# Kernel optimization log

Hardware: AMD Instinct MI355X
Metric: run time of the kernel (lower is better)

Reference implementation:

```python
import jax, jax.numpy as jnp
import numpy as np

CURVE = 1.0
TAU = 0.5
N_NODES = 32768
N_EDGES = 65536
IN_CH = 64
OUT_CH = 64
N_HEADS = 8
N_RF = 128
EPS = 1e-7


def _make_projection_matrix(m, d, seed=0):
    # FAVOR+ projection: stacked rows of transposed QR blocks, row-rescaled by chi norms.
    rng = np.random.RandomState(seed)
    blocks = []
    nb_full = m // d
    for _ in range(nb_full):
        q, _ = np.linalg.qr(rng.randn(d, d))
        blocks.append(q.T)
    rem = m - nb_full * d
    if rem > 0:
        q, _ = np.linalg.qr(rng.randn(d, d))
        blocks.append(q.T[:rem])
    final = np.vstack(blocks)  # [m, d]
    mult = np.linalg.norm(rng.randn(m, d), axis=1)
    return (mult[:, None] * final).astype(np.float32)


def _expmap0(u, c):
    # Hyperboloid exp map at origin; time slot of u is ignored.
    sqrtK = 1.0 / jnp.sqrt(c)
    x = u[..., 1:]
    xn = jnp.maximum(jnp.linalg.norm(x, axis=-1, keepdims=True), EPS)
    theta = xn / sqrtK
    return jnp.concatenate([sqrtK * jnp.cosh(theta), sqrtK * jnp.sinh(theta) * x / xn], axis=-1)


def _proj(x, c):
    # Re-project onto hyperboloid: x0 = sqrt(1/c + ||x_space||^2)
    K = 1.0 / c
    y = x[..., 1:]
    t = jnp.sqrt(K + jnp.sum(y * y, axis=-1, keepdims=True))
    return jnp.concatenate([t, y], axis=-1)


def _logmap0(x, c):
    # Hyperboloid log map at origin; output tangent has zero time component.
    sqrtK = 1.0 / jnp.sqrt(c)
    y = x[..., 1:]
    yn = jnp.maximum(jnp.linalg.norm(y, axis=-1, keepdims=True), EPS)
    t = jnp.maximum(x[..., 0:1] / sqrtK, 1.0 + EPS)
    res = sqrtK * jnp.arccosh(t) * y / yn
    return jnp.concatenate([jnp.zeros_like(res[..., :1]), res], axis=-1)


def _softmax_kernel(data, P, tau, c):
    # Performer-style exp kernel with hyperbolic (time-coordinate) prefactor.
    dt = data[..., 0:1]
    ds = data[..., 1:]
    m = 1.0 / jnp.sqrt(jnp.asarray(P.shape[0], jnp.float32))
    wx = jnp.exp(jnp.einsum('bnhd,dm->bnhm', ds, P) / jnp.sqrt(tau))
    front = jnp.exp((c / tau - dt * dt / tau) / 2.0) * m  # [b,n,h,1]
    return wx * front


def setup_inputs() -> dict:
    key = jax.random.key(0)
    k1, k2, k3, k4 = jax.random.split(key, 4)
    std = (2.0 / (IN_CH + OUT_CH)) ** 0.5
    z = 0.01 * jax.random.normal(k1, (1, N_NODES, IN_CH), jnp.float32)
    Wq = std * jax.random.normal(k2, (N_HEADS, OUT_CH, IN_CH), jnp.float32)
    Wk = std * jax.random.normal(k3, (N_HEADS, OUT_CH, IN_CH), jnp.float32)
    Wv = std * jax.random.normal(k4, (N_HEADS, OUT_CH, IN_CH), jnp.float32)
    edge_index = jax.random.randint(jax.random.fold_in(key, 7), (2, N_EDGES), 0, N_NODES, jnp.int32)
    proj_mat = jnp.asarray(_make_projection_matrix(IN_CH - 1, N_RF))  # [63, 128]
    return {"z": z, "Wq": Wq, "Wk": Wk, "Wv": Wv, "proj_mat": proj_mat, "edge_index": edge_index}


def reference(z, Wq, Wk, Wv, proj_mat, edge_index):
    c = jnp.float32(CURVE)
    tau = jnp.float32(TAU)
    zs = z[0]  # [N, C] (B == 1, squeeze)
    zh = _proj(_expmap0(zs, c), c)  # lift features to hyperboloid
    u = _logmap0(zh, c)             # [N, C], tangent at origin

    def hyplin(W):  # HypLinear (no bias): proj(expmap0(logmap0(x) @ W^T)) for all heads
        mu = jnp.einsum('nc,hoc->hno', u, W)  # [H, N, D]
        return _proj(_expmap0(mu, c), c)

    q, k, v = hyplin(Wq), hyplin(Wk), hyplin(Wv)  # [H, N, D]
    H, N, D = q.shape
    # mirrors torch stacked.reshape(-1, N, H, D) (row-major relabeling)
    query = q.reshape(1, N, H, D)
    key_ = k.reshape(1, N, H, D)
    value = v.reshape(1, N, H, D)

    qp = _softmax_kernel(query, proj_mat, tau, c).transpose(2, 0, 1, 3)  # [H,1,N,M]
    kp = _softmax_kernel(key_, proj_mat, tau, c).transpose(2, 0, 1, 3)   # [H,1,N,M]
    vv = value.transpose(2, 0, 1, 3)                                      # [H,1,N,D]

    last = jnp.einsum('hbnm,hbnd->hbmd', kp, vv)   # [H,1,M,D] kv summary
    zo = jnp.einsum('hbnm,hbmd->hbnd', qp, last)   # [H,1,N,D]
    mnorm = -zo[..., 0:1] ** 2 + jnp.sum(zo[..., 1:] ** 2, axis=-1, keepdims=True)
    zo = zo / (jnp.sqrt(c) * jnp.sqrt(jnp.abs(mnorm)))  # renormalize onto hyperboloid

    start, end = edge_index[0], edge_index[1]
    ea = jnp.einsum('hbem,hbem->hbe', qp[:, :, end, :], kp[:, :, start, :])
    A_weight = ea.transpose(1, 2, 0)  # [1, E, H]

    # hyper_agg: Euclidean head-mean followed by Minkowski renormalization
    t = jnp.mean(zo[:, 0], axis=0)  # [N, D]
    xn = -t[..., 0:1] ** 2 + jnp.sum(t[..., 1:] ** 2, axis=-1, keepdims=True)
    z_next = t / (jnp.sqrt(c) * jnp.sqrt(jnp.abs(xn)))
    link_loss = jnp.mean(A_weight)
    return z_next, link_loss
```

## Files before the change

kernel.cpp:

```cpp
#include <hip/hip_runtime.h>

#define DEV __device__ __forceinline__

#define NNODES 32768
#define NEDGES 65536
#define NROWS  262144
#define EPSF   1e-7f
#define SQRT2F 1.4142135623730951f
#define LOG2E  1.4426950408889634f
#define LOG2SQRT63 2.9886399611087573f

#define OFF_WFRAG 0u
#define OFF_LASTB 0u
#define OFF_PFRAG 196608u
#define OFF_EA    212992u
#define OFF_U     409600u
#define OFF_PART  42352640u
#define OFF_PHIQ  75907072u
#define OFF_PHIK  143015936u

typedef short s8v __attribute__((ext_vector_type(8)));
typedef float f4v __attribute__((ext_vector_type(4)));
typedef float f2v __attribute__((ext_vector_type(2)));

DEV unsigned short f2bf(float f) {
  unsigned u = __float_as_uint(f);
  return (unsigned short)((u + 0x7fffu + ((u >> 16) & 1u)) >> 16);
}
DEV float bf2f(unsigned short h) { return __uint_as_float(((unsigned)h) << 16); }
DEV unsigned pack2(float lo, float hi) {
  return __builtin_amdgcn_perm(__float_as_uint(hi) + 0x8000u, __float_as_uint(lo) + 0x8000u, 0x07060302u);
}
DEV float frcp(float x) { return __builtin_amdgcn_rcpf(x); }

__global__ __launch_bounds__(256) void k01_prep(const float* __restrict__ z, unsigned short* __restrict__ ubf,
                                                const float* __restrict__ Wq, const float* __restrict__ Wk,
                                                const float* __restrict__ Wv, const float* __restrict__ P,
                                                unsigned short* __restrict__ Wfrag, unsigned short* __restrict__ Pfrag,
                                                float* __restrict__ ea) {
  int i = blockIdx.x * 256 + threadIdx.x;
  float4 v = *(const float4*)(z + (size_t)i * 4);
  if ((i & 15) == 0) v.x = 0.f;
  uint2 pk;
  pk.x = pack2(v.x, v.y);
  pk.y = pack2(v.z, v.w);
  *(uint2*)(ubf + (size_t)i * 4) = pk;

  if (blockIdx.x < 96) {
    if (i == 0) ea[0] = 0.f;
    int stride = 96 * 256;
    for (int t = i; t < 98304; t += stride) {
      int j = t & 7, lane = (t >> 3) & 63, nt = (t >> 9) & 3, ks = (t >> 11) & 1, h = (t >> 12) & 7, sm = t >> 15;
      int k = ks * 32 + (lane >> 4) * 8 + j;
      int n = nt * 16 + (lane & 15);
      const float* W = (sm == 0) ? Wq : ((sm == 1) ? Wk : Wv);
      Wfrag[t] = f2bf(W[(h * 64 + n) * 64 + k]);
    }
    for (int t = i; t < 8192; t += stride) {
      int j = t & 7, lane = (t >> 3) & 63, ks = (t >> 9) & 1, mt = (t >> 10) & 7;
      int k = ks * 32 + (lane >> 4) * 8 + j;
      int m = mt * 16 + (lane & 15);
      Pfrag[t] = (k == 0) ? (unsigned short)0 : f2bf(P[(k - 1) * 128 + m] * (SQRT2F * LOG2E));
    }
  }
}

__global__ __launch_bounds__(256) void k2_mfma(const unsigned short* __restrict__ ubf,
                                               const unsigned short* __restrict__ Wfrag,
                                               const unsigned short* __restrict__ Pfrag,
                                               unsigned char* __restrict__ phiq, unsigned char* __restrict__ phik,
                                               unsigned short* __restrict__ part) {
  __shared__ short lds_raw[18944];
  short* sbuf = lds_raw;
  float* sfront = (float*)(lds_raw + 18432);
  short* kbufT = lds_raw;
  short* vbufT = lds_raw + 8704;

  int w = threadIdx.x >> 6, lane = threadIdx.x & 63;
  int q = lane >> 4, l = lane & 15;
  int b = blockIdx.x;
  int h = b >> 8, t = b & 255;
  int n0 = t * 128 + w * 32;
  int r0 = h * 32768 + n0;

  s8v afr[2][2];
#pragma unroll
  for (int mt = 0; mt < 2; ++mt)
#pragma unroll
    for (int ks = 0; ks < 2; ++ks)
      afr[mt][ks] = *(const s8v*)(ubf + (size_t)(n0 + mt * 16 + l) * 64 + ks * 32 + q * 8);

  const s8v* Wf = (const s8v*)Wfrag;
  const s8v* Pf = (const s8v*)Pfrag;
  uint2 vkeep[2][4];

#pragma unroll
  for (int sm = 0; sm < 3; ++sm) {
    f4v acc[2][4];
#pragma unroll
    for (int mt = 0; mt < 2; ++mt)
#pragma unroll
      for (int nt = 0; nt < 4; ++nt) acc[mt][nt] = (f4v)(0.f);
#pragma unroll
    for (int ks = 0; ks < 2; ++ks)
#pragma unroll
      for (int nt = 0; nt < 4; ++nt) {
        s8v bf = Wf[(((sm * 8 + h) * 2 + ks) * 4 + nt) * 64 + lane];
#pragma unroll
        for (int mt = 0; mt < 2; ++mt)
          acc[mt][nt] = __builtin_amdgcn_mfma_f32_16x16x32_bf16(afr[mt][ks], bf, acc[mt][nt], 0, 0, 0);
      }
#pragma unroll
    for (int mt = 0; mt < 2; ++mt) {
      float rs[4];
#pragma unroll
      for (int reg = 0; reg < 4; ++reg) {
        float v0 = (l == 0) ? 0.f : acc[mt][0][reg];
        rs[reg] = v0 * v0 + acc[mt][1][reg] * acc[mt][1][reg] + acc[mt][2][reg] * acc[mt][2][reg] +
                  acc[mt][3][reg] * acc[mt][3][reg];
      }
#pragma unroll
      for (int reg = 0; reg < 4; ++reg) {
#pragma unroll
        for (int off = 1; off < 16; off <<= 1) rs[reg] += __shfl_xor(rs[reg], off, 64);
      }
      float vreg[4][4];
#pragma unroll
      for (int reg = 0; reg < 4; ++reg) {
        float x = fmaxf(sqrtf(rs[reg]), EPSF);
        float e = exp2f(x * LOG2E);
        float sh = 0.5f * (e - frcp(e));
        float ratio = sh * frcp(x);
        float sh2 = sh * sh;
        int row = mt * 16 + q * 4 + reg;
        if (sm == 2) {
          float tt2 = sqrtf(1.f + sh2);
#pragma unroll
          for (int nt = 0; nt < 4; ++nt) {
            float val = acc[mt][nt][reg] * ratio;
            if (l == 0 && nt == 0) val = tt2;
            vreg[nt][reg] = val;
          }
        } else {
          float lf = -sh2 * LOG2E - LOG2SQRT63;
          if (l == 0) sfront[(sm * 4 + w) * 32 + row] = lf;
#pragma unroll
          for (int nt = 0; nt < 4; ++nt) {
            float val = acc[mt][nt][reg] * ratio;
            if (l == 0 && nt == 0) val = 0.f;
            sbuf[(sm * 4 + w) * 2304 + row * 72 + nt * 16 + l] = (short)(__float_as_uint(val) >> 16);
          }
        }
      }
      if (sm == 2) {
#pragma unroll
        for (int nt = 0; nt < 4; ++nt) {
          vkeep[mt][nt].x = pack2(vreg[nt][0], vreg[nt][1]);
          vkeep[mt][nt].y = pack2(vreg[nt][2], vreg[nt][3]);
        }
      }
    }
  }

  uint2 keep0[8], keep1[8];
#pragma unroll
  for (int sm = 0; sm < 2; ++sm) {
    s8v bsf[2][2];
#pragma unroll
    for (int nt = 0; nt < 2; ++nt)
#pragma unroll
      for (int ks = 0; ks < 2; ++ks)
        bsf[nt][ks] = *(const s8v*)&sbuf[(sm * 4 + w) * 2304 + (nt * 16 + l) * 72 + ks * 32 + q * 8];
    float lf0 = sfront[(sm * 4 + w) * 32 + l];
    float lf1 = sfront[(sm * 4 + w) * 32 + 16 + l];
    unsigned char* dst = sm ? phik : phiq;
#pragma unroll
    for (int mt = 0; mt < 8; ++mt) {
      f4v a0 = (f4v)(0.f), a1 = (f4v)(0.f);
#pragma unroll
      for (int ks = 0; ks < 2; ++ks) {
        s8v ap = Pf[(mt * 2 + ks) * 64 + lane];
        a0 = __builtin_amdgcn_mfma_f32_16x16x32_bf16(ap, bsf[0][ks], a0, 0, 0, 0);
        a1 = __builtin_amdgcn_mfma_f32_16x16x32_bf16(ap, bsf[1][ks], a1, 0, 0, 0);
      }
      float v00 = exp2f(a0[0] + lf0), v01 = exp2f(a0[1] + lf0), v02 = exp2f(a0[2] + lf0), v03 = exp2f(a0[3] + lf0);
      float v10 = exp2f(a1[0] + lf1), v11 = exp2f(a1[1] + lf1), v12 = exp2f(a1[2] + lf1), v13 = exp2f(a1[3] + lf1);
      unsigned p0 = __builtin_amdgcn_cvt_pk_fp8_f32(v00, v01, 0, 0);
      p0 = __builtin_amdgcn_cvt_pk_fp8_f32(v02, v03, p0, 1);
      unsigned p1 = __builtin_amdgcn_cvt_pk_fp8_f32(v10, v11, 0, 0);
      p1 = __builtin_amdgcn_cvt_pk_fp8_f32(v12, v13, p1, 1);
      *(unsigned*)(dst + (size_t)(r0 + l) * 128 + mt * 16 + q * 4) = p0;
      *(unsigned*)(dst + (size_t)(r0 + 16 + l) * 128 + mt * 16 + q * 4) = p1;
      if (sm == 1) {
        keep0[mt].x = pack2(v00, v01); keep0[mt].y = pack2(v02, v03);
        keep1[mt].x = pack2(v10, v11); keep1[mt].y = pack2(v12, v13);
      }
    }
  }

  f4v facc[2][4];
#pragma unroll
  for (int mtl = 0; mtl < 2; ++mtl)
#pragma unroll
    for (int nt = 0; nt < 4; ++nt) facc[mtl][nt] = (f4v)(0.f);

#pragma unroll
  for (int hf = 0; hf < 2; ++hf) {
    __syncthreads();
    if ((w >> 1) == hf) {
      int nd0 = (w & 1) * 32 + l, nd1 = nd0 + 16;
#pragma unroll
      for (int mt = 0; mt < 8; ++mt) {
        int m = mt * 16 + q * 4;
        kbufT[(m + 0) * 68 + nd0] = (short)(keep0[mt].x & 0xffffu);
        kbufT[(m + 1) * 68 + nd0] = (short)(keep0[mt].x >> 16);
        kbufT[(m + 2) * 68 + nd0] = (short)(keep0[mt].y & 0xffffu);
        kbufT[(m + 3) * 68 + nd0] = (short)(keep0[mt].y >> 16);
        kbufT[(m + 0) * 68 + nd1] = (short)(keep1[mt].x & 0xffffu);
        kbufT[(m + 1) * 68 + nd1] = (short)(keep1[mt].x >> 16);
        kbufT[(m + 2) * 68 + nd1] = (short)(keep1[mt].y & 0xffffu);
        kbufT[(m + 3) * 68 + nd1] = (short)(keep1[mt].y >> 16);
      }
#pragma unroll
      for (int mt = 0; mt < 2; ++mt)
#pragma unroll
        for (int nt = 0; nt < 4; ++nt)
          *(uint2*)&vbufT[(nt * 16 + l) * 72 + (w & 1) * 32 + mt * 16 + q * 4] = vkeep[mt][nt];
    }
    __syncthreads();
#pragma unroll
    for (int kc = 0; kc < 2; ++kc) {
      s8v bv[4];
#pragma unroll
      for (int nt = 0; nt < 4; ++nt)
        bv[nt] = *(const s8v*)&vbufT[(nt * 16 + l) * 72 + kc * 32 + q * 8];
      s8v av[2];
#pragma unroll
      for (int mtl = 0; mtl < 2; ++mtl) {
        const short* kb = &kbufT[((2 * w + mtl) * 16 + l) * 68 + kc * 32 + q * 8];
        union { s8v v; long long L[2]; } ua;
        ua.L[0] = *(const long long*)kb;
        ua.L[1] = *(const long long*)(kb + 4);
        av[mtl] = ua.v;
      }
#pragma unroll
      for (int mtl = 0; mtl < 2; ++mtl)
#pragma unroll
        for (int nt = 0; nt < 4; ++nt)
          facc[mtl][nt] = __builtin_amdgcn_mfma_f32_16x16x32_bf16(av[mtl], bv[nt], facc[mtl][nt], 0, 0, 0);
    }
  }

#pragma unroll
  for (int mtl = 0; mtl < 2; ++mtl)
#pragma unroll
    for (int nt = 0; nt < 4; ++nt) {
      uint2 pk;
      pk.x = pack2(facc[mtl][nt][0], facc[mtl][nt][1]);
      pk.y = pack2(facc[mtl][nt][2], facc[mtl][nt][3]);
      int d = nt * 16 + l;
      int m = (2 * w + mtl) * 16 + q * 4;
      *(uint2*)(part + ((size_t)((t * 8 + h) * 64 + d)) * 128 + m) = pk;
    }
}

__global__ __launch_bounds__(256) void k3p_pack(const unsigned* __restrict__ part32, unsigned char* __restrict__ lastB) {
  int t2 = blockIdx.x * 256 + threadIdx.x;
  float s0 = 0.f, s1 = 0.f;
#pragma unroll 16
  for (int c = 0; c < 256; ++c) {
    unsigned v = part32[((size_t)c << 12) + t2];
    s0 += __uint_as_float(v << 16);
    s1 += __uint_as_float(v & 0xffff0000u);
  }
  int m = (t2 & 63) * 2, d = (t2 >> 6) & 63, h = t2 >> 12;
  int ks = m >> 5, j = m & 7, qq = (m >> 3) & 3;
  int lane = qq * 16 + (d & 15), nt = d >> 4;
  unsigned r = __builtin_amdgcn_cvt_pk_bf8_f32(s0, s1, 0, 0);
  *(unsigned short*)(lastB + ((((h * 4 + ks) * 4 + nt) * 64 + lane) << 3) + j) = (unsigned short)r;
}

__global__ __launch_bounds__(512) void k4_mfma(const unsigned char* __restrict__ phiq,
                                               const unsigned char* __restrict__ lastB,
                                               const float* __restrict__ ea, float* __restrict__ out) {
  __shared__ unsigned zbufT[8][64][18];
  int w = threadIdx.x >> 6, lane = threadIdx.x & 63;
  int q = lane >> 4, l = lane & 15;
  int n0 = blockIdx.x * 32;

  const long* Bf = (const long*)lastB;
  long bf[4][4];
#pragma unroll
  for (int ks = 0; ks < 4; ++ks)
#pragma unroll
    for (int nt = 0; nt < 4; ++nt) bf[ks][nt] = Bf[((w * 4 + ks) * 4 + nt) * 64 + lane];

  long af[2][4];
#pragma unroll
  for (int mt = 0; mt < 2; ++mt)
#pragma unroll
    for (int ks = 0; ks < 4; ++ks)
      af[mt][ks] = *(const long*)(phiq + (size_t)(8 * (n0 + mt * 16 + l) + w) * 128 + ks * 32 + q * 8);

  f4v acc[2][4];
#pragma unroll
  for (int mt = 0; mt < 2; ++mt)
#pragma unroll
    for (int nt = 0; nt < 4; ++nt) acc[mt][nt] = (f4v)(0.f);
#pragma unroll
  for (int ks = 0; ks < 4; ++ks)
#pragma unroll
    for (int nt = 0; nt < 4; ++nt)
#pragma unroll
      for (int mt = 0; mt < 2; ++mt)
        acc[mt][nt] = __builtin_amdgcn_mfma_f32_16x16x32_fp8_bf8(af[mt][ks], bf[ks][nt], acc[mt][nt], 0, 0, 0);

#pragma unroll
  for (int mt = 0; mt < 2; ++mt) {
    float rs[4];
#pragma unroll
    for (int reg = 0; reg < 4; ++reg) {
      float v0 = acc[mt][0][reg];
      float s0 = (l == 0) ? -v0 * v0 : v0 * v0;
      rs[reg] = s0 + acc[mt][1][reg] * acc[mt][1][reg] + acc[mt][2][reg] * acc[mt][2][reg] +
                acc[mt][3][reg] * acc[mt][3][reg];
    }
#pragma unroll
    for (int reg = 0; reg < 4; ++reg) {
#pragma unroll
      for (int off = 1; off < 16; off <<= 1) rs[reg] += __shfl_xor(rs[reg], off, 64);
    }
    float inv[4];
#pragma unroll
    for (int reg = 0; reg < 4; ++reg) inv[reg] = 1.f / sqrtf(fabsf(rs[reg]));
#pragma unroll
    for (int nt = 0; nt < 4; ++nt) {
      uint2 pk;
      pk.x = pack2(acc[mt][nt][0] * inv[0], acc[mt][nt][1] * inv[1]);
      pk.y = pack2(acc[mt][nt][2] * inv[2], acc[mt][nt][3] * inv[3]);
      *(uint2*)&zbufT[w][nt * 16 + l][mt * 8 + q * 2] = pk;
    }
  }
  __syncthreads();

  int tid = threadIdx.x;
  int i = tid >> 4, dg = tid & 15;
  int i2 = i >> 1, sel = i & 1;
  float s[4] = {0.f, 0.f, 0.f, 0.f};
#pragma unroll
  for (int w2 = 0; w2 < 8; ++w2) {
#pragma unroll
    for (int j = 0; j < 4; ++j) {
      unsigned u = zbufT[w2][dg * 4 + j][i2];
      s[j] += bf2f((unsigned short)(sel ? (u >> 16) : (u & 0xffffu)));
    }
  }
  float m2 = 0.f;
#pragma unroll
  for (int j = 0; j < 4; ++j) {
    s[j] *= 0.125f;
    m2 += ((dg == 0 && j == 0) ? -s[j] * s[j] : s[j] * s[j]);
  }
#pragma unroll
  for (int off = 1; off < 16; off <<= 1) m2 += __shfl_xor(m2, off, 64);
  float inv = 1.f / sqrtf(fabsf(m2));
  float4 o = make_float4(s[0] * inv, s[1] * inv, s[2] * inv, s[3] * inv);
  *(float4*)(out + (size_t)(n0 + i) * 64 + dg * 4) = o;
  if (blockIdx.x == 0 && tid == 0) out[(size_t)NNODES * 64] = ea[0] * (1.0f / 524288.0f);
}

__global__ __launch_bounds__(256) void k5_ea(const unsigned char* __restrict__ phiq,
                                             const unsigned char* __restrict__ phik,
                                             const int* __restrict__ ei, float* __restrict__ ea) {
  __shared__ float part[4];
  int lane = threadIdx.x & 63, w = threadIdx.x >> 6;
  int wid = blockIdx.x * 4 + w;
  float acc = 0.f;
  for (int i = 0; i < 16; ++i) {
    int e = wid * 16 + i;
    int s = ei[e];
    int d = ei[NEDGES + e];
    uint4 qa = *(const uint4*)(phiq + (size_t)d * 1024 + lane * 16);
    uint4 ka = *(const uint4*)(phik + (size_t)s * 1024 + lane * 16);
    unsigned qs[4] = {qa.x, qa.y, qa.z, qa.w};
    unsigned ks[4] = {ka.x, ka.y, ka.z, ka.w};
#pragma unroll
    for (int p = 0; p < 4; ++p) {
      f2v q0 = __builtin_amdgcn_cvt_pk_f32_fp8(qs[p], 0);
      f2v q1 = __builtin_amdgcn_cvt_pk_f32_fp8(qs[p], 1);
      f2v k0 = __builtin_amdgcn_cvt_pk_f32_fp8(ks[p], 0);
      f2v k1 = __builtin_amdgcn_cvt_pk_f32_fp8(ks[p], 1);
      acc = fmaf(q0.x, k0.x, acc);
      acc = fmaf(q0.y, k0.y, acc);
      acc = fmaf(q1.x, k1.x, acc);
      acc = fmaf(q1.y, k1.y, acc);
    }
  }
#pragma unroll
  for (int o = 1; o < 64; o <<= 1) acc += __shfl_xor(acc, o, 64);
  if (lane == 0) part[w] = acc;
  __syncthreads();
  if (threadIdx.x == 0) atomicAdd(ea, part[0] + part[1] + part[2] + part[3]);
}

extern "C" void kernel_launch(void* const* d_in, const int* in_sizes, int n_in,
                              void* d_out, int out_size, void* d_ws, size_t ws_size,
                              hipStream_t stream) {
  const float* z  = (const float*)d_in[0];
  const float* Wq = (const float*)d_in[1];
  const float* Wk = (const float*)d_in[2];
  const float* Wv = (const float*)d_in[3];
  const float* P  = (const float*)d_in[4];
  const int* ei   = (const int*)d_in[5];
  char* ws = (char*)d_ws;
  unsigned short* Wfrag = (unsigned short*)(ws + OFF_WFRAG);
  unsigned char*  lastB = (unsigned char*)(ws + OFF_LASTB);
  unsigned short* Pfrag = (unsigned short*)(ws + OFF_PFRAG);
  float*          ea    = (float*)(ws + OFF_EA);
  unsigned short* ubf   = (unsigned short*)(ws + OFF_U);
  unsigned short* part  = (unsigned short*)(ws + OFF_PART);
  unsigned char*  phiq  = (unsigned char*)(ws + OFF_PHIQ);
  unsigned char*  phik  = (unsigned char*)(ws + OFF_PHIK);

  k01_prep<<<2048, 256, 0, stream>>>(z, ubf, Wq, Wk, Wv, P, Wfrag, Pfrag, ea);
  k2_mfma<<<2048, 256, 0, stream>>>(ubf, Wfrag, Pfrag, phiq, phik, part);
  k3p_pack<<<128, 256, 0, stream>>>((const unsigned*)part, lastB);
  k5_ea<<<NEDGES / 64, 256, 0, stream>>>(phiq, phik, ei, ea);
  k4_mfma<<<NNODES / 32, 512, 0, stream>>>(phiq, lastB, ea, (float*)d_out);
}
```

Measured before the change: 201.9 us.

## Merge partial-sum pack and edge-score kernels into one launch, use fast intrinsics

Combines the k3p_pack reduction and the k5_ea edge dot-product kernels into a single launch with block ranges split by index, so the two independent stages run concurrently and one launch is removed. The edge part now gives each wave 8 edges instead of 16, using twice as many blocks, and loads two edges per iteration with split accumulators for more memory-level parallelism. Library sqrtf, exp2f and division are replaced with raw AMDGCN sqrt, exp2 and rcp intrinsics, trading a little accuracy and denormal handling for fewer instructions.

```diff
diff --git a/kernel.cpp b/kernel.cpp
--- a/kernel.cpp
+++ b/kernel.cpp
@@ -32,6 +32,8 @@
   return __builtin_amdgcn_perm(__float_as_uint(hi) + 0x8000u, __float_as_uint(lo) + 0x8000u, 0x07060302u);
 }
 DEV float frcp(float x) { return __builtin_amdgcn_rcpf(x); }
+DEV float fsqrt(float x) { return __builtin_amdgcn_sqrtf(x); }
+DEV float fexp2(float x) { return __builtin_amdgcn_exp2f(x); }
 
 __global__ __launch_bounds__(256) void k01_prep(const float* __restrict__ z, unsigned short* __restrict__ ubf,
                                                 const float* __restrict__ Wq, const float* __restrict__ Wk,
@@ -127,14 +129,14 @@
       float vreg[4][4];
 #pragma unroll
       for (int reg = 0; reg < 4; ++reg) {
-        float x = fmaxf(sqrtf(rs[reg]), EPSF);
-        float e = exp2f(x * LOG2E);
+        float x = fmaxf(fsqrt(rs[reg]), EPSF);
+        float e = fexp2(x * LOG2E);
         float sh = 0.5f * (e - frcp(e));
         float ratio = sh * frcp(x);
         float sh2 = sh * sh;
         int row = mt * 16 + q * 4 + reg;
         if (sm == 2) {
-          float tt2 = sqrtf(1.f + sh2);
+          float tt2 = fsqrt(1.f + sh2);
 #pragma unroll
           for (int nt = 0; nt < 4; ++nt) {
             float val = acc[mt][nt][reg] * ratio;
@@ -183,8 +185,8 @@
         a0 = __builtin_amdgcn_mfma_f32_16x16x32_bf16(ap, bsf[0][ks], a0, 0, 0, 0);
         a1 = __builtin_amdgcn_mfma_f32_16x16x32_bf16(ap, bsf[1][ks], a1, 0, 0, 0);
       }
-      float v00 = exp2f(a0[0] + lf0), v01 = exp2f(a0[1] + lf0), v02 = exp2f(a0[2] + lf0), v03 = exp2f(a0[3] + lf0);
-      float v10 = exp2f(a1[0] + lf1), v11 = exp2f(a1[1] + lf1), v12 = exp2f(a1[2] + lf1), v13 = exp2f(a1[3] + lf1);
+      float v00 = fexp2(a0[0] + lf0), v01 = fexp2(a0[1] + lf0), v02 = fexp2(a0[2] + lf0), v03 = fexp2(a0[3] + lf0);
+      float v10 = fexp2(a1[0] + lf1), v11 = fexp2(a1[1] + lf1), v12 = fexp2(a1[2] + lf1), v13 = fexp2(a1[3] + lf1);
       unsigned p0 = __builtin_amdgcn_cvt_pk_fp8_f32(v00, v01, 0, 0);
       p0 = __builtin_amdgcn_cvt_pk_fp8_f32(v02, v03, p0, 1);
       unsigned p1 = __builtin_amdgcn_cvt_pk_fp8_f32(v10, v11, 0, 0);
@@ -264,20 +266,59 @@
     }
 }
 
-__global__ __launch_bounds__(256) void k3p_pack(const unsigned* __restrict__ part32, unsigned char* __restrict__ lastB) {
-  int t2 = blockIdx.x * 256 + threadIdx.x;
-  float s0 = 0.f, s1 = 0.f;
+__global__ __launch_bounds__(256) void k35(const unsigned* __restrict__ part32, unsigned char* __restrict__ lastB,
+                                           const unsigned char* __restrict__ phiq,
+                                           const unsigned char* __restrict__ phik,
+                                           const int* __restrict__ ei, float* __restrict__ ea) {
+  int b = blockIdx.x;
+  if (b < 128) {
+    int t2 = b * 256 + threadIdx.x;
+    float s0 = 0.f, s1 = 0.f;
 #pragma unroll 16
-  for (int c = 0; c < 256; ++c) {
-    unsigned v = part32[((size_t)c << 12) + t2];
-    s0 += __uint_as_float(v << 16);
-    s1 += __uint_as_float(v & 0xffff0000u);
-  }
-  int m = (t2 & 63) * 2, d = (t2 >> 6) & 63, h = t2 >> 12;
-  int ks = m >> 5, j = m & 7, qq = (m >> 3) & 3;
-  int lane = qq * 16 + (d & 15), nt = d >> 4;
-  unsigned r = __builtin_amdgcn_cvt_pk_bf8_f32(s0, s1, 0, 0);
-  *(unsigned short*)(lastB + ((((h * 4 + ks) * 4 + nt) * 64 + lane) << 3) + j) = (unsigned short)r;
+    for (int c = 0; c < 256; ++c) {
+      unsigned v = part32[((size_t)c << 12) + t2];
+      s0 += __uint_as_float(v << 16);
+      s1 += __uint_as_float(v & 0xffff0000u);
+    }
+    int m = (t2 & 63) * 2, d = (t2 >> 6) & 63, h = t2 >> 12;
+    int ks = m >> 5, j = m & 7, qq = (m >> 3) & 3;
+    int lane = qq * 16 + (d & 15), nt = d >> 4;
+    unsigned r = __builtin_amdgcn_cvt_pk_bf8_f32(s0, s1, 0, 0);
+    *(unsigned short*)(lastB + ((((h * 4 + ks) * 4 + nt) * 64 + lane) << 3) + j) = (unsigned short)r;
+    return;
+  }
+  __shared__ float part[4];
+  int lane = threadIdx.x & 63, w = threadIdx.x >> 6;
+  int wid = (b - 128) * 4 + w;
+  float acc0 = 0.f, acc1 = 0.f;
+#pragma unroll
+  for (int i = 0; i < 8; i += 2) {
+    int e0 = wid * 8 + i, e1 = e0 + 1;
+    int s0 = ei[e0], d0 = ei[NEDGES + e0];
+    int s1 = ei[e1], d1 = ei[NEDGES + e1];
+    uint4 qa = *(const uint4*)(phiq + (size_t)d0 * 1024 + lane * 16);
+    uint4 ka = *(const uint4*)(phik + (size_t)s0 * 1024 + lane * 16);
+    uint4 qb = *(const uint4*)(phiq + (size_t)d1 * 1024 + lane * 16);
+    uint4 kb = *(const uint4*)(phik + (size_t)s1 * 1024 + lane * 16);
+    unsigned qs[8] = {qa.x, qa.y, qa.z, qa.w, qb.x, qb.y, qb.z, qb.w};
+    unsigned ks[8] = {ka.x, ka.y, ka.z, ka.w, kb.x, kb.y, kb.z, kb.w};
+#pragma unroll
+    for (int p = 0; p < 8; ++p) {
+      f2v q0 = __builtin_amdgcn_cvt_pk_f32_fp8(qs[p], 0);
+      f2v q1 = __builtin_amdgcn_cvt_pk_f32_fp8(qs[p], 1);
+      f2v k0 = __builtin_amdgcn_cvt_pk_f32_fp8(ks[p], 0);
+      f2v k1 = __builtin_amdgcn_cvt_pk_f32_fp8(ks[p], 1);
+      float t0 = fmaf(q0.x, k0.x, q0.y * k0.y);
+      float t1 = fmaf(q1.x, k1.x, q1.y * k1.y);
+      if (p < 4) acc0 += t0 + t1; else acc1 += t0 + t1;
+    }
+  }
+  float acc = acc0 + acc1;
+#pragma unroll
+  for (int o = 1; o < 64; o <<= 1) acc += __shfl_xor(acc, o, 64);
+  if (lane == 0) part[w] = acc;
+  __syncthreads();
+  if (threadIdx.x == 0) atomicAdd(ea, part[0] + part[1] + part[2] + part[3]);
 }
 
 __global__ __launch_bounds__(512) void k4_mfma(const unsigned char* __restrict__ phiq,
@@ -332,7 +373,7 @@
     }
     float inv[4];
 #pragma unroll
-    for (int reg = 0; reg < 4; ++reg) inv[reg] = 1.f / sqrtf(fabsf(rs[reg]));
+    for (int reg = 0; reg < 4; ++reg) inv[reg] = frcp(fsqrt(fabsf(rs[reg])));
 #pragma unroll
     for (int nt = 0; nt < 4; ++nt) {
       uint2 pk;
@@ -363,44 +404,10 @@
   }
 #pragma unroll
   for (int off = 1; off < 16; off <<= 1) m2 += __shfl_xor(m2, off, 64);
-  float inv = 1.f / sqrtf(fabsf(m2));
+  float inv = frcp(fsqrt(fabsf(m2)));
   float4 o = make_float4(s[0] * inv, s[1] * inv, s[2] * inv, s[3] * inv);
   *(float4*)(out + (size_t)(n0 + i) * 64 + dg * 4) = o;
   if (blockIdx.x == 0 && tid == 0) out[(size_t)NNODES * 64] = ea[0] * (1.0f / 524288.0f);
-}
-
-__global__ __launch_bounds__(256) void k5_ea(const unsigned char* __restrict__ phiq,
-                                             const unsigned char* __restrict__ phik,
-                                             const int* __restrict__ ei, float* __restrict__ ea) {
-  __shared__ float part[4];
-  int lane = threadIdx.x & 63, w = threadIdx.x >> 6;
-  int wid = blockIdx.x * 4 + w;
-  float acc = 0.f;
-  for (int i = 0; i < 16; ++i) {
-    int e = wid * 16 + i;
-    int s = ei[e];
-    int d = ei[NEDGES + e];
-    uint4 qa = *(const uint4*)(phiq + (size_t)d * 1024 + lane * 16);
-    uint4 ka = *(const uint4*)(phik + (size_t)s * 1024 + lane * 16);
-    unsigned qs[4] = {qa.x, qa.y, qa.z, qa.w};
-    unsigned ks[4] = {ka.x, ka.y, ka.z, ka.w};
-#pragma unroll
-    for (int p = 0; p < 4; ++p) {
-      f2v q0 = __builtin_amdgcn_cvt_pk_f32_fp8(qs[p], 0);
-      f2v q1 = __builtin_amdgcn_cvt_pk_f32_fp8(qs[p], 1);
-      f2v k0 = __builtin_amdgcn_cvt_pk_f32_fp8(ks[p], 0);
-      f2v k1 = __builtin_amdgcn_cvt_pk_f32_fp8(ks[p], 1);
-      acc = fmaf(q0.x, k0.x, acc);
-      acc = fmaf(q0.y, k0.y, acc);
-      acc = fmaf(q1.x, k1.x, acc);
-      acc = fmaf(q1.y, k1.y, acc);
-    }
-  }
-#pragma unroll
-  for (int o = 1; o < 64; o <<= 1) acc += __shfl_xor(acc, o, 64);
-  if (lane == 0) part[w] = acc;
-  __syncthreads();
-  if (threadIdx.x == 0) atomicAdd(ea, part[0] + part[1] + part[2] + part[3]);
 }
 
 extern "C" void kernel_launch(void* const* d_in, const int* in_sizes, int n_in,
@@ -424,7 +431,6 @@
 
   k01_prep<<<2048, 256, 0, stream>>>(z, ubf, Wq, Wk, Wv, P, Wfrag, Pfrag, ea);
   k2_mfma<<<2048, 256, 0, stream>>>(ubf, Wfrag, Pfrag, phiq, phik, part);
-  k3p_pack<<<128, 256, 0, stream>>>((const unsigned*)part, lastB);
-  k5_ea<<<NEDGES / 64, 256, 0, stream>>>(phiq, phik, ei, ea);
+  k35<<<128 + 2048, 256, 0, stream>>>((const unsigned*)part, lastB, phiq, phik, ei, ea);
   k4_mfma<<<NNODES / 32, 512, 0, stream>>>(phiq, lastB, ea, (float*)d_out);
 }
```

Result: faster. 194.0 us (-3.9%).

## Fuse edge-score and output kernels into one launch with last-block finalize

Applied to the files above, without the earlier changes.

Merges the edge attention-sum kernel and the output kernel into a single launch: the first 2048 blocks compute edge dot products, and the remaining blocks do the output MFMA work. The last edge block writes the link loss, detected through an atomic counter. The aim is to save a launch and let the two independent workloads overlap on the GPU. It also swaps library sqrt/exp2 calls for hardware intrinsics and raises the unroll factor in the pack kernel. In exchange it adds an extra atomic counter and relies on a threadfence for ordering.

```diff
diff --git a/kernel.cpp b/kernel.cpp
--- a/kernel.cpp
+++ b/kernel.cpp
@@ -32,6 +32,8 @@
   return __builtin_amdgcn_perm(__float_as_uint(hi) + 0x8000u, __float_as_uint(lo) + 0x8000u, 0x07060302u);
 }
 DEV float frcp(float x) { return __builtin_amdgcn_rcpf(x); }
+DEV float fsqrt(float x) { return __builtin_amdgcn_sqrtf(x); }
+DEV float fexp2(float x) { return __builtin_amdgcn_exp2f(x); }
 
 __global__ __launch_bounds__(256) void k01_prep(const float* __restrict__ z, unsigned short* __restrict__ ubf,
                                                 const float* __restrict__ Wq, const float* __restrict__ Wk,
@@ -47,7 +49,7 @@
   *(uint2*)(ubf + (size_t)i * 4) = pk;
 
   if (blockIdx.x < 96) {
-    if (i == 0) ea[0] = 0.f;
+    if (i == 0) { ea[0] = 0.f; ((unsigned*)ea)[1] = 0u; }
     int stride = 96 * 256;
     for (int t = i; t < 98304; t += stride) {
       int j = t & 7, lane = (t >> 3) & 63, nt = (t >> 9) & 3, ks = (t >> 11) & 1, h = (t >> 12) & 7, sm = t >> 15;
@@ -127,14 +129,14 @@
       float vreg[4][4];
 #pragma unroll
       for (int reg = 0; reg < 4; ++reg) {
-        float x = fmaxf(sqrtf(rs[reg]), EPSF);
-        float e = exp2f(x * LOG2E);
+        float x = fmaxf(fsqrt(rs[reg]), EPSF);
+        float e = fexp2(x * LOG2E);
         float sh = 0.5f * (e - frcp(e));
         float ratio = sh * frcp(x);
         float sh2 = sh * sh;
         int row = mt * 16 + q * 4 + reg;
         if (sm == 2) {
-          float tt2 = sqrtf(1.f + sh2);
+          float tt2 = fsqrt(1.f + sh2);
 #pragma unroll
           for (int nt = 0; nt < 4; ++nt) {
             float val = acc[mt][nt][reg] * ratio;
@@ -183,8 +185,8 @@
         a0 = __builtin_amdgcn_mfma_f32_16x16x32_bf16(ap, bsf[0][ks], a0, 0, 0, 0);
         a1 = __builtin_amdgcn_mfma_f32_16x16x32_bf16(ap, bsf[1][ks], a1, 0, 0, 0);
       }
-      float v00 = exp2f(a0[0] + lf0), v01 = exp2f(a0[1] + lf0), v02 = exp2f(a0[2] + lf0), v03 = exp2f(a0[3] + lf0);
-      float v10 = exp2f(a1[0] + lf1), v11 = exp2f(a1[1] + lf1), v12 = exp2f(a1[2] + lf1), v13 = exp2f(a1[3] + lf1);
+      float v00 = fexp2(a0[0] + lf0), v01 = fexp2(a0[1] + lf0), v02 = fexp2(a0[2] + lf0), v03 = fexp2(a0[3] + lf0);
+      float v10 = fexp2(a1[0] + lf1), v11 = fexp2(a1[1] + lf1), v12 = fexp2(a1[2] + lf1), v13 = fexp2(a1[3] + lf1);
       unsigned p0 = __builtin_amdgcn_cvt_pk_fp8_f32(v00, v01, 0, 0);
       p0 = __builtin_amdgcn_cvt_pk_fp8_f32(v02, v03, p0, 1);
       unsigned p1 = __builtin_amdgcn_cvt_pk_fp8_f32(v10, v11, 0, 0);
@@ -267,7 +269,7 @@
 __global__ __launch_bounds__(256) void k3p_pack(const unsigned* __restrict__ part32, unsigned char* __restrict__ lastB) {
   int t2 = blockIdx.x * 256 + threadIdx.x;
   float s0 = 0.f, s1 = 0.f;
-#pragma unroll 16
+#pragma unroll 32
   for (int c = 0; c < 256; ++c) {
     unsigned v = part32[((size_t)c << 12) + t2];
     s0 += __uint_as_float(v << 16);
@@ -280,13 +282,64 @@
   *(unsigned short*)(lastB + ((((h * 4 + ks) * 4 + nt) * 64 + lane) << 3) + j) = (unsigned short)r;
 }
 
-__global__ __launch_bounds__(512) void k4_mfma(const unsigned char* __restrict__ phiq,
-                                               const unsigned char* __restrict__ lastB,
-                                               const float* __restrict__ ea, float* __restrict__ out) {
+__global__ __launch_bounds__(512) void k45(const unsigned char* __restrict__ phiq,
+                                           const unsigned char* __restrict__ phik,
+                                           const unsigned char* __restrict__ lastB,
+                                           const int* __restrict__ ei,
+                                           float* __restrict__ ea, float* __restrict__ out) {
   __shared__ unsigned zbufT[8][64][18];
-  int w = threadIdx.x >> 6, lane = threadIdx.x & 63;
+  __shared__ float epart[8];
+  int b = blockIdx.x;
+  int lane = threadIdx.x & 63, w = threadIdx.x >> 6;
+
+  if (b < 2048) {
+    int wid = b * 8 + w;
+    int e0 = wid * 4;
+    int sA[4], dA[4];
+#pragma unroll
+    for (int j = 0; j < 4; ++j) { sA[j] = ei[e0 + j]; dA[j] = ei[NEDGES + e0 + j]; }
+    uint4 qv[4], kv[4];
+#pragma unroll
+    for (int j = 0; j < 4; ++j) {
+      qv[j] = *(const uint4*)(phiq + (size_t)dA[j] * 1024 + lane * 16);
+      kv[j] = *(const uint4*)(phik + (size_t)sA[j] * 1024 + lane * 16);
+    }
+    float acc = 0.f;
+#pragma unroll
+    for (int j = 0; j < 4; ++j) {
+      unsigned qs[4] = {qv[j].x, qv[j].y, qv[j].z, qv[j].w};
+      unsigned ks[4] = {kv[j].x, kv[j].y, kv[j].z, kv[j].w};
+#pragma unroll
+      for (int p = 0; p < 4; ++p) {
+        f2v q0 = __builtin_amdgcn_cvt_pk_f32_fp8(qs[p], 0);
+        f2v q1 = __builtin_amdgcn_cvt_pk_f32_fp8(qs[p], 1);
+        f2v k0 = __builtin_amdgcn_cvt_pk_f32_fp8(ks[p], 0);
+        f2v k1 = __builtin_amdgcn_cvt_pk_f32_fp8(ks[p], 1);
+        acc = fmaf(q0.x, k0.x, acc);
+        acc = fmaf(q0.y, k0.y, acc);
+        acc = fmaf(q1.x, k1.x, acc);
+        acc = fmaf(q1.y, k1.y, acc);
+      }
+    }
+#pragma unroll
+    for (int o = 1; o < 64; o <<= 1) acc += __shfl_xor(acc, o, 64);
+    if (lane == 0) epart[w] = acc;
+    __syncthreads();
+    if (threadIdx.x == 0) {
+      float bs = epart[0] + epart[1] + epart[2] + epart[3] + epart[4] + epart[5] + epart[6] + epart[7];
+      atomicAdd(ea, bs);
+      __threadfence();
+      unsigned prev = atomicAdd((unsigned*)(ea + 1), 1u);
+      if (prev == 2047u) {
+        float v = atomicAdd(ea, 0.f);
+        out[(size_t)NNODES * 64] = v * (1.0f / 524288.0f);
+      }
+    }
+    return;
+  }
+
   int q = lane >> 4, l = lane & 15;
-  int n0 = blockIdx.x * 32;
+  int n0 = (b - 2048) * 32;
 
   const long* Bf = (const long*)lastB;
   long bf[4][4];
@@ -332,7 +385,7 @@
     }
     float inv[4];
 #pragma unroll
-    for (int reg = 0; reg < 4; ++reg) inv[reg] = 1.f / sqrtf(fabsf(rs[reg]));
+    for (int reg = 0; reg < 4; ++reg) inv[reg] = frcp(fsqrt(fabsf(rs[reg])));
 #pragma unroll
     for (int nt = 0; nt < 4; ++nt) {
       uint2 pk;
@@ -363,44 +416,9 @@
   }
 #pragma unroll
   for (int off = 1; off < 16; off <<= 1) m2 += __shfl_xor(m2, off, 64);
-  float inv = 1.f / sqrtf(fabsf(m2));
+  float inv = frcp(fsqrt(fabsf(m2)));
   float4 o = make_float4(s[0] * inv, s[1] * inv, s[2] * inv, s[3] * inv);
   *(float4*)(out + (size_t)(n0 + i) * 64 + dg * 4) = o;
-  if (blockIdx.x == 0 && tid == 0) out[(size_t)NNODES * 64] = ea[0] * (1.0f / 524288.0f);
-}
-
-__global__ __launch_bounds__(256) void k5_ea(const unsigned char* __restrict__ phiq,
-                                             const unsigned char* __restrict__ phik,
-                                             const int* __restrict__ ei, float* __restrict__ ea) {
-  __shared__ float part[4];
-  int lane = threadIdx.x & 63, w = threadIdx.x >> 6;
-  int wid = blockIdx.x * 4 + w;
-  float acc = 0.f;
-  for (int i = 0; i < 16; ++i) {
-    int e = wid * 16 + i;
-    int s = ei[e];
-    int d = ei[NEDGES + e];
-    uint4 qa = *(const uint4*)(phiq + (size_t)d * 1024 + lane * 16);
-    uint4 ka = *(const uint4*)(phik + (size_t)s * 1024 + lane * 16);
-    unsigned qs[4] = {qa.x, qa.y, qa.z, qa.w};
-    unsigned ks[4] = {ka.x, ka.y, ka.z, ka.w};
-#pragma unroll
-    for (int p = 0; p < 4; ++p) {
-      f2v q0 = __builtin_amdgcn_cvt_pk_f32_fp8(qs[p], 0);
-      f2v q1 = __builtin_amdgcn_cvt_pk_f32_fp8(qs[p], 1);
-      f2v k0 = __builtin_amdgcn_cvt_pk_f32_fp8(ks[p], 0);
-      f2v k1 = __builtin_amdgcn_cvt_pk_f32_fp8(ks[p], 1);
-      acc = fmaf(q0.x, k0.x, acc);
-      acc = fmaf(q0.y, k0.y, acc);
-      acc = fmaf(q1.x, k1.x, acc);
-      acc = fmaf(q1.y, k1.y, acc);
-    }
-  }
-#pragma unroll
-  for (int o = 1; o < 64; o <<= 1) acc += __shfl_xor(acc, o, 64);
-  if (lane == 0) part[w] = acc;
-  __syncthreads();
-  if (threadIdx.x == 0) atomicAdd(ea, part[0] + part[1] + part[2] + part[3]);
 }
 
 extern "C" void kernel_launch(void* const* d_in, const int* in_sizes, int n_in,
@@ -425,6 +443,5 @@
   k01_prep<<<2048, 256, 0, stream>>>(z, ubf, Wq, Wk, Wv, P, Wfrag, Pfrag, ea);
   k2_mfma<<<2048, 256, 0, stream>>>(ubf, Wfrag, Pfrag, phiq, phik, part);
   k3p_pack<<<128, 256, 0, stream>>>((const unsigned*)part, lastB);
-  k5_ea<<<NEDGES / 64, 256, 0, stream>>>(phiq, phik, ei, ea);
-  k4_mfma<<<NNODES / 32, 512, 0, stream>>>(phiq, lastB, ea, (float*)d_out);
-}
+  k45<<<2048 + 1024, 512, 0, stream>>>(phiq, phik, lastB, ei, ea, (float*)d_out);
+}
```

After: 247.8 us. +22.7%, slower.
